# Optimization experiments

Measured on AMD Instinct MI355X. Metric: run time of the kernel, lower is better.

The kernel has to match this reference:

```python
import jax
import jax.numpy as jnp
import numpy as np

N_NODES = 4096
N_EDGES = 65536
D_FEAT = 64


def setup_inputs() -> dict:
    key = jax.random.key(0)
    k1, k2, k3, k4 = jax.random.split(key, 4)
    x = jax.random.normal(k1, (N_NODES, D_FEAT), dtype=jnp.float32)
    edge_index = jax.random.randint(k2, (2, N_EDGES), 0, N_NODES, dtype=jnp.int32)
    batch = jnp.zeros((N_NODES,), dtype=jnp.int32)
    # GraphConv(in_channels, 1): lin_rel (with bias) on aggregated neighbors, lin_root on self
    w_rel = jax.random.normal(k3, (D_FEAT, 1), dtype=jnp.float32) * 0.1
    w_root = jax.random.normal(k4, (D_FEAT, 1), dtype=jnp.float32) * 0.1
    b = jnp.zeros((1,), dtype=jnp.float32)
    return {"x": x, "edge_index": edge_index, "batch": batch,
            "w_rel": w_rel, "w_root": w_root, "b": b}


def _merge_stars(x, src0, dst0, score):
    """Faithful sequential greedy star contraction (priority order by score desc)."""
    N = x.shape[0]
    order = jnp.argsort(-score)  # descending, ties like argsort

    def step(carry, node):
        xc, src, dst, remaining, center = carry
        active = remaining[node]
        # dests = set of targets of edges whose (current, rewritten) source == node,
        # minus already-chosen center nodes
        dest_edge = src == node                                  # [E]
        dest_node = jnp.zeros(N, bool).at[dst].max(dest_edge)    # node-level set
        dest_node = dest_node & ~center
        # torch does sum over list(dests)+[node]: node counted again (even on self-loop)
        combine = jnp.einsum('n,nd->d', dest_node.astype(xc.dtype), xc) + xc[node]
        D = dest_node.at[node].set(True)                         # dests U {node}
        x2 = xc.at[node].set(combine)
        src2 = jnp.where(D[src], node, src)                      # np.isin rewrite
        dst2 = jnp.where(D[dst], node, dst)
        rem2 = remaining & ~dest_node
        cen2 = center.at[node].set(True)
        carry2 = (jnp.where(active, x2, xc),
                  jnp.where(active, src2, src),
                  jnp.where(active, dst2, dst),
                  jnp.where(active, rem2, remaining),
                  jnp.where(active, cen2, center))
        return carry2, None

    init = (x, src0, dst0, jnp.ones(N, bool), jnp.zeros(N, bool))
    (x_final, _, _, remaining, _), _ = jax.lax.scan(step, init, order)
    return x_final, remaining


def reference(x, edge_index, batch, w_rel, w_root, b):
    N, d = x.shape
    src0, dst0 = edge_index[0], edge_index[1]
    # GraphConv score: W_rel * sum_{j->i} x_j + b + W_root * x_i ; dropout p=0; tanh
    agg = jax.ops.segment_sum(x[src0], dst0, num_segments=N)     # [N, d]
    score = jnp.tanh((agg @ w_rel + x @ w_root + b).reshape(-1)) # [N]

    x_final, remaining = _merge_stars(x, src0, dst0, score)

    # perm = sorted(nodes_remaining); outputs padded to static size N (sentinel -1)
    perm = jnp.nonzero(remaining, size=N, fill_value=N)[0]
    x_pooled = jnp.take(x_final, perm, axis=0, mode='fill', fill_value=0.0)
    kept = perm < N
    batch_pooled = jnp.where(kept, jnp.take(batch, jnp.minimum(perm, N - 1)), -1)
    # filter_adj on the ORIGINAL edge_index: keep edges with both endpoints kept,
    # relabel nodes to their rank among kept nodes; invalid edges -> -1
    relabel = jnp.cumsum(remaining.astype(jnp.int32)) - 1
    valid = remaining[src0] & remaining[dst0]
    new_src = jnp.where(valid, relabel[src0], -1)
    new_dst = jnp.where(valid, relabel[dst0], -1)
    new_edge_index = jnp.stack([new_src, new_dst])
    perm_out = jnp.where(kept, perm, -1)
    return x_pooled, new_edge_index, batch_pooled, perm_out
```

## Files before the change

### kernel.cpp

```cpp
#include <hip/hip_runtime.h>

#define NN 4096
#define NE 65536
#define ND 64


__global__ void __launch_bounds__(1024) kB_csr(const int* __restrict__ ei,
                                               unsigned short* __restrict__ incsr_g,
                                               int* __restrict__ rowst_g) {
    __shared__ __align__(16) char buf[147520];
    unsigned short* incsr = (unsigned short*)buf;
    int* cursor = (int*)(buf + 131072);
    int* wt = (int*)(buf + 147456);
    int tid = threadIdx.x, lane = tid & 63, wv = tid >> 6;

    for (int n = tid; n < NN; n += 1024) cursor[n] = 0;
    __syncthreads();
    const int4* eid4 = (const int4*)(ei + NE);
    for (int i = tid; i < NE / 4; i += 1024) {
        int4 q = eid4[i];
        atomicAdd(&cursor[q.x], 1);
        atomicAdd(&cursor[q.y], 1);
        atomicAdd(&cursor[q.z], 1);
        atomicAdd(&cursor[q.w], 1);
    }
    __syncthreads();

    int t0 = cursor[4 * tid], t1 = cursor[4 * tid + 1];
    int t2 = cursor[4 * tid + 2], t3 = cursor[4 * tid + 3];
    int tot = t0 + t1 + t2 + t3;
    int inc = tot;
    for (int off = 1; off < 64; off <<= 1) {
        int v = __shfl_up(inc, off);
        if (lane >= off) inc += v;
    }
    if (lane == 63) wt[wv] = inc;
    __syncthreads();
    if (wv == 0 && lane < 16) {
        int v = wt[lane];
        for (int off = 1; off < 16; off <<= 1) {
            int u2 = __shfl_up(v, off);
            if (lane >= off) v += u2;
        }
        wt[lane] = v;
    }
    __syncthreads();
    int waveoff = (wv > 0) ? wt[wv - 1] : 0;
    int excl = waveoff + inc - tot;
    int4 rsv;
    rsv.x = excl; rsv.y = excl + t0; rsv.z = excl + t0 + t1; rsv.w = excl + t0 + t1 + t2;
    ((int4*)rowst_g)[tid] = rsv;
    if (tid == 1023) rowst_g[NN] = NE;
    cursor[4 * tid]     = rsv.x;
    cursor[4 * tid + 1] = rsv.y;
    cursor[4 * tid + 2] = rsv.z;
    cursor[4 * tid + 3] = rsv.w;
    __syncthreads();

    const int4* eis4 = (const int4*)ei;
    for (int i = tid; i < NE / 4; i += 1024) {
        int4 s = eis4[i];
        int4 d = eid4[i];
        incsr[atomicAdd(&cursor[d.x], 1)] = (unsigned short)s.x;
        incsr[atomicAdd(&cursor[d.y], 1)] = (unsigned short)s.y;
        incsr[atomicAdd(&cursor[d.z], 1)] = (unsigned short)s.z;
        incsr[atomicAdd(&cursor[d.w], 1)] = (unsigned short)s.w;
    }
    __syncthreads();

    for (int i = tid; i < 8192; i += 1024)
        ((int4*)incsr_g)[i] = ((const int4*)incsr)[i];
}

__global__ void kX_keys(const float* __restrict__ x, const float* __restrict__ wrel,
                        const float* __restrict__ wroot, const float* __restrict__ bptr,
                        const int* __restrict__ rowst, const unsigned short* __restrict__ incsr,
                        unsigned* __restrict__ key) {
    int gt = blockIdx.x * blockDim.x + threadIdx.x;
    int v = gt >> 6, lane = gt & 63;
    int rs = rowst[v], deg = rowst[v + 1] - rs;
    double acc = 0.0;
    for (int base = 0; base < deg; base += 64) {
        int n = deg - base; if (n > 64) n = 64;
        int ent = (lane < n) ? (int)incsr[rs + base + lane] : 0;
        for (int e = 0; e < n; ++e) {
            int u = __shfl(ent, e);
            acc += (double)x[(u << 6) | lane];
        }
    }
    double red = acc * (double)wrel[lane]
               + (double)x[(v << 6) | lane] * (double)wroot[lane];
    for (int off = 32; off > 0; off >>= 1) red += __shfl_down(red, off);
    if (lane == 0) {
        float sc = tanhf((float)(red + (double)bptr[0]));
        unsigned m = __float_as_uint(sc);
        m = (m & 0x80000000u) ? ~m : (m | 0x80000000u);
        key[v] = m;
    }
}

__global__ void k5_filtersort(const int* __restrict__ rowst, const unsigned* __restrict__ key,
                              unsigned short* __restrict__ incsr, int* __restrict__ rl,
                              float* __restrict__ out) {
    int g = blockIdx.x * blockDim.x + threadIdx.x;
    if (g < (NN * ND) / 4) ((float4*)out)[g] = make_float4(0.f, 0.f, 0.f, 0.f);

    int v = g >> 6, l = g & 63;
    int rs = rowst[v], deg = rowst[v + 1] - rs;
    unsigned mv = key[v];
    if (deg <= 64) {
        int u = (l < deg) ? (int)incsr[rs + l] : -1;
        bool isself = (l < deg) && (u == v);
        unsigned mu = (l < deg && !isself) ? key[u] : 0u;
        bool keep = (l < deg) && !isself && (mu > mv || (mu == mv && u < v));
        unsigned long long val = keep
            ? ((((unsigned long long)(~mu)) << 12) | (unsigned)u) : ~0ULL;
        int m = __popcll(__ballot(keep));
        bool selfAny = __ballot(isself) != 0ULL;
        for (int k = 2; k <= 64; k <<= 1) {
            for (int j = k >> 1; j > 0; j >>= 1) {
                unsigned long long o = __shfl_xor(val, j);
                bool takeMin = ((l & k) == 0) == ((l & j) == 0);
                unsigned long long mn = (o < val) ? o : val;
                unsigned long long mx = (o < val) ? val : o;
                val = takeMin ? mn : mx;
            }
        }
        if (l < m) incsr[rs + l] = (unsigned short)(val & 0xFFFULL);
        if (l == 0) rl[v] = m | (selfAny ? 0x10000 : 0);
    } else if (l == 0) {
        int w = rs;
        bool selfAny = false;
        for (int e = rs; e < rs + deg; ++e) {
            int u = (int)incsr[e];
            if (u == v) { selfAny = true; continue; }
            unsigned mu = key[u];
            if (!(mu > mv || (mu == mv && u < v))) continue;
            int j = w;
            while (j > rs) {
                int q = (int)incsr[j - 1];
                unsigned mq = key[q];
                if (mu > mq || (mu == mq && u < q)) { incsr[j] = (unsigned short)q; --j; }
                else break;
            }
            incsr[j] = (unsigned short)u; ++w;
        }
        rl[v] = (w - rs) | (selfAny ? 0x10000 : 0);
    }
}

__global__ void __launch_bounds__(1024) k34_fix(
        const int* __restrict__ rowst, const int* __restrict__ rl,
        const unsigned short* __restrict__ incsr_g,
        int* __restrict__ map_g, int* __restrict__ rem_g, int* __restrict__ relab_g,
        int* __restrict__ perm_a, int* __restrict__ nkeep_g) {
    __shared__ __align__(16) char buf[135232];
    unsigned short* incsr = (unsigned short*)buf;
    volatile unsigned char* stat = (volatile unsigned char*)(buf + 131072);
    int* wt = (int*)(buf + 135168);
    int tid = threadIdx.x, lane = tid & 63, wv = tid >> 6;

    for (int i = tid; i < 131072 / 16; i += 1024)
        ((int4*)incsr)[i] = ((const int4*)incsr_g)[i];
    ((int*)(buf + 131072))[tid] = 0;
    int4 rsq = ((const int4*)rowst)[tid];
    int4 rlq = ((const int4*)rl)[tid];
    int rs4[4] = {rsq.x, rsq.y, rsq.z, rsq.w};
    int rq4[4] = {rlq.x, rlq.y, rlq.z, rlq.w};
    __syncthreads();

    unsigned resolved = 0, centerm = 0, selfm = 0;
    int pos4[4], re4[4], fu4[4] = {0, 0, 0, 0};
    #pragma unroll
    for (int t = 0; t < 4; ++t) {
        int v = 4 * tid + t;
        int m = rq4[t] & 0xFFFF;
        if (rq4[t] & 0x10000) selfm |= 1u << t;
        int lo = rs4[t];
        pos4[t] = lo; re4[t] = lo + m;
        if (m == 0) {
            map_g[v] = v; stat[v] = 1;
            centerm |= 1u << t; resolved |= 1u << t;
        } else {
            fu4[t] = (int)incsr[lo];
        }
    }

    int guard = 0;
    while (resolved != 0xFu && guard < 1000000) {
        ++guard;
        bool prog = false;
        #pragma unroll
        for (int t = 0; t < 4; ++t) {
            if (resolved & (1u << t)) continue;
            int v = 4 * tid + t;
            int u = fu4[t];
            int st = (int)stat[u];
            if (st == 0) continue;
            prog = true;
            if (st == 1) {
                map_g[v] = u; stat[v] = 2; resolved |= 1u << t; continue;
            }
            int p = pos4[t] + 1, hi = re4[t];
            bool done = false;
            while (p < hi) {
                u = (int)incsr[p];
                st = (int)stat[u];
                if (st == 2) { ++p; continue; }
                if (st == 1) {
                    map_g[v] = u; stat[v] = 2; resolved |= 1u << t; done = true;
                }
                break;
            }
            if (!done) {
                if (p >= hi) {
                    map_g[v] = v; stat[v] = 1; centerm |= 1u << t; resolved |= 1u << t;
                } else {
                    pos4[t] = p; fu4[t] = u;
                }
            }
        }
        if (__ballot(prog) == 0) __builtin_amdgcn_s_sleep(1);
    }
    __syncthreads();

    int remb[4], cnt4 = 0;
    #pragma unroll
    for (int t = 0; t < 4; ++t) {
        remb[t] = ((centerm >> t) & 1) && !((selfm >> t) & 1);
        cnt4 += remb[t];
    }
    int inc2 = cnt4;
    for (int off = 1; off < 64; off <<= 1) {
        int v = __shfl_up(inc2, off);
        if (lane >= off) inc2 += v;
    }
    if (lane == 63) wt[wv] = inc2;
    __syncthreads();
    if (wv == 0 && lane < 16) {
        int v = wt[lane];
        for (int off = 1; off < 16; off <<= 1) {
            int u2 = __shfl_up(v, off);
            if (lane >= off) v += u2;
        }
        wt[lane] = v;
    }
    __syncthreads();
    int woff2 = (wv > 0) ? wt[wv - 1] : 0;
    int run = woff2 + inc2 - cnt4;
    #pragma unroll
    for (int t = 0; t < 4; ++t) {
        int v = 4 * tid + t;
        relab_g[v] = run;
        if (remb[t]) { perm_a[run] = v; ++run; }
        rem_g[v] = remb[t];
    }
    if (tid == 1023) nkeep_g[0] = run;
}

__global__ void k56_outputs(const float* __restrict__ x, const int* __restrict__ map_g,
                            const int* __restrict__ rem_g, const int* __restrict__ relab_g,
                            const int* __restrict__ perm_a, const int* __restrict__ ei,
                            const int* __restrict__ batch, const int* __restrict__ nkeep_g,
                            float* __restrict__ out) {
    int idx = blockIdx.x * blockDim.x + threadIdx.x;
    if (idx < NN * ND) {
        int n = idx >> 6, d = idx & 63;
        int m = map_g[n];
        if (rem_g[m]) atomicAdd(&out[relab_g[m] * ND + d], x[idx]);
    } else if (idx < NN * ND + 2 * NE) {
        int e = idx - NN * ND;
        int row = e >> 16;
        int ee = e & (NE - 1);
        int s = ei[ee], t = ei[NE + ee];
        bool valid = (rem_g[s] != 0) && (rem_g[t] != 0);
        int endp = (row == 0) ? s : t;
        out[idx] = valid ? (float)relab_g[endp] : -1.0f;
    } else if (idx < NN * ND + 2 * NE + NN) {
        int r = idx - (NN * ND + 2 * NE);
        int nk = nkeep_g[0];
        out[idx] = (r < nk) ? (float)batch[perm_a[r]] : -1.0f;
    } else if (idx < NN * ND + 2 * NE + 2 * NN) {
        int r = idx - (NN * ND + 2 * NE + NN);
        int nk = nkeep_g[0];
        out[idx] = (r < nk) ? (float)perm_a[r] : -1.0f;
    }
}

extern "C" void kernel_launch(void* const* d_in, const int* in_sizes, int n_in,
                              void* d_out, int out_size, void* d_ws, size_t ws_size,
                              hipStream_t stream) {
    const float* x     = (const float*)d_in[0];
    const int*   ei    = (const int*)d_in[1];
    const int*   batch = (const int*)d_in[2];
    const float* wrel  = (const float*)d_in[3];
    const float* wroot = (const float*)d_in[4];
    const float* b     = (const float*)d_in[5];

    char* ws = (char*)d_ws;
    int*    map_g  = (int*)(ws + 0);
    int*    rem_g  = (int*)(ws + 16384);
    int*    relab  = (int*)(ws + 32768);
    int*    perma  = (int*)(ws + 49152);
    int*    nkeep  = (int*)(ws + 65536);
    int*    rl     = (int*)(ws + 65600);
    int*    rowst  = (int*)(ws + 81984);
    unsigned* key  = (unsigned*)(ws + 98432);
    unsigned short* incsr = (unsigned short*)(ws + 114816);

    float* out = (float*)d_out;

    kB_csr<<<1, 1024, 0, stream>>>(ei, incsr, rowst);
    kX_keys<<<1024, 256, 0, stream>>>(x, wrel, wroot, b, rowst, incsr, key);
    k5_filtersort<<<1024, 256, 0, stream>>>(rowst, key, incsr, rl, out);
    k34_fix<<<1, 1024, 0, stream>>>(rowst, rl, incsr, map_g, rem_g, relab, perma, nkeep);
    int total_out = NN * ND + 2 * NE + 2 * NN;
    k56_outputs<<<(total_out + 255) / 256, 256, 0, stream>>>(x, map_g, rem_g, relab,
                                                             perma, ei, batch, nkeep, out);
}
```

Measured before the change: 140.1 us.

## Assign nodes to threads in priority-rank order for the star-resolution loop

k5_filtersort now also computes each node's global rank by score, using a full wave-wide count over all 4096 keys per node, and writes it to a new workspace buffer. k34_fix builds a rank-to-node table in shared memory and maps nodes to threads in priority order. Higher-priority nodes, whose decisions others wait on, then sit in earlier threads and waves, which is meant to shorten the spin-wait dependency chain in the single-block loop. The cost is extra L2 traffic for the rank count, more shared memory, and a degree field packed into 7 bits that relies on small kept degrees.

```diff
diff --git a/kernel.cpp b/kernel.cpp
--- a/kernel.cpp
+++ b/kernel.cpp
@@ -101,7 +101,7 @@
 
 __global__ void k5_filtersort(const int* __restrict__ rowst, const unsigned* __restrict__ key,
                               unsigned short* __restrict__ incsr, int* __restrict__ rl,
-                              float* __restrict__ out) {
+                              int* __restrict__ rank_g, float* __restrict__ out) {
     int g = blockIdx.x * blockDim.x + threadIdx.x;
     if (g < (NN * ND) / 4) ((float4*)out)[g] = make_float4(0.f, 0.f, 0.f, 0.f);
 
@@ -147,17 +147,36 @@
         }
         rl[v] = (w - rs) | (selfAny ? 0x10000 : 0);
     }
+
+    {
+        int cntk = 0;
+        const uint4* k4p = (const uint4*)key;
+        #pragma unroll 4
+        for (int i = 0; i < 16; ++i) {
+            uint4 kq = k4p[(l << 4) | i];
+            int u0 = (l << 6) | (i << 2);
+            cntk += (kq.x > mv || (kq.x == mv && (u0    ) < v));
+            cntk += (kq.y > mv || (kq.y == mv && (u0 + 1) < v));
+            cntk += (kq.z > mv || (kq.z == mv && (u0 + 2) < v));
+            cntk += (kq.w > mv || (kq.w == mv && (u0 + 3) < v));
+        }
+        for (int off = 32; off > 0; off >>= 1) cntk += __shfl_down(cntk, off);
+        if (l == 0) rank_g[v] = cntk;
+    }
 }
 
 __global__ void __launch_bounds__(1024) k34_fix(
         const int* __restrict__ rowst, const int* __restrict__ rl,
-        const unsigned short* __restrict__ incsr_g,
+        const unsigned short* __restrict__ incsr_g, const int* __restrict__ rank_g,
         int* __restrict__ map_g, int* __restrict__ rem_g, int* __restrict__ relab_g,
         int* __restrict__ perm_a, int* __restrict__ nkeep_g) {
-    __shared__ __align__(16) char buf[135232];
+    __shared__ __align__(16) char buf[155776];
     unsigned short* incsr = (unsigned short*)buf;
     volatile unsigned char* stat = (volatile unsigned char*)(buf + 131072);
-    int* wt = (int*)(buf + 135168);
+    unsigned short* r2n = (unsigned short*)(buf + 135168);
+    unsigned short* rst = (unsigned short*)(buf + 143360);
+    unsigned char*  lsf = (unsigned char*)(buf + 151552);
+    int* wt = (int*)(buf + 155648);
     int tid = threadIdx.x, lane = tid & 63, wv = tid >> 6;
 
     for (int i = tid; i < 131072 / 16; i += 1024)
@@ -165,22 +184,31 @@
     ((int*)(buf + 131072))[tid] = 0;
     int4 rsq = ((const int4*)rowst)[tid];
     int4 rlq = ((const int4*)rl)[tid];
-    int rs4[4] = {rsq.x, rsq.y, rsq.z, rsq.w};
-    int rq4[4] = {rlq.x, rlq.y, rlq.z, rlq.w};
-    __syncthreads();
-
-    unsigned resolved = 0, centerm = 0, selfm = 0;
-    int pos4[4], re4[4], fu4[4] = {0, 0, 0, 0};
+    int4 rkq = ((const int4*)rank_g)[tid];
+    int rs4s[4] = {rsq.x, rsq.y, rsq.z, rsq.w};
+    int rq4s[4] = {rlq.x, rlq.y, rlq.z, rlq.w};
+    int rk4s[4] = {rkq.x, rkq.y, rkq.z, rkq.w};
     #pragma unroll
     for (int t = 0; t < 4; ++t) {
         int v = 4 * tid + t;
-        int m = rq4[t] & 0xFFFF;
-        if (rq4[t] & 0x10000) selfm |= 1u << t;
-        int lo = rs4[t];
+        rst[v] = (unsigned short)rs4s[t];
+        lsf[v] = (unsigned char)((rq4s[t] & 0x7F) | ((rq4s[t] & 0x10000) ? 0x80 : 0));
+        r2n[rk4s[t]] = (unsigned short)v;
+    }
+    __syncthreads();
+
+    unsigned resolved = 0;
+    int pos4[4], re4[4], fu4[4] = {0, 0, 0, 0}, vr4[4];
+    #pragma unroll
+    for (int t = 0; t < 4; ++t) {
+        int v = (int)r2n[4 * tid + t];
+        vr4[t] = v;
+        int lo = (int)rst[v];
+        int m = lsf[v] & 0x7F;
         pos4[t] = lo; re4[t] = lo + m;
         if (m == 0) {
             map_g[v] = v; stat[v] = 1;
-            centerm |= 1u << t; resolved |= 1u << t;
+            resolved |= 1u << t;
         } else {
             fu4[t] = (int)incsr[lo];
         }
@@ -193,7 +221,7 @@
         #pragma unroll
         for (int t = 0; t < 4; ++t) {
             if (resolved & (1u << t)) continue;
-            int v = 4 * tid + t;
+            int v = vr4[t];
             int u = fu4[t];
             int st = (int)stat[u];
             if (st == 0) continue;
@@ -214,7 +242,7 @@
             }
             if (!done) {
                 if (p >= hi) {
-                    map_g[v] = v; stat[v] = 1; centerm |= 1u << t; resolved |= 1u << t;
+                    map_g[v] = v; stat[v] = 1; resolved |= 1u << t;
                 } else {
                     pos4[t] = p; fu4[t] = u;
                 }
@@ -227,7 +255,8 @@
     int remb[4], cnt4 = 0;
     #pragma unroll
     for (int t = 0; t < 4; ++t) {
-        remb[t] = ((centerm >> t) & 1) && !((selfm >> t) & 1);
+        int v = 4 * tid + t;
+        remb[t] = (stat[v] == 1) && !(lsf[v] & 0x80);
         cnt4 += remb[t];
     }
     int inc2 = cnt4;
@@ -306,14 +335,16 @@
     int*    rl     = (int*)(ws + 65600);
     int*    rowst  = (int*)(ws + 81984);
     unsigned* key  = (unsigned*)(ws + 98432);
-    unsigned short* incsr = (unsigned short*)(ws + 114816);
+    int*    rankp  = (int*)(ws + 114816);
+    unsigned short* incsr = (unsigned short*)(ws + 131200);
 
     float* out = (float*)d_out;
 
     kB_csr<<<1, 1024, 0, stream>>>(ei, incsr, rowst);
     kX_keys<<<1024, 256, 0, stream>>>(x, wrel, wroot, b, rowst, incsr, key);
-    k5_filtersort<<<1024, 256, 0, stream>>>(rowst, key, incsr, rl, out);
-    k34_fix<<<1, 1024, 0, stream>>>(rowst, rl, incsr, map_g, rem_g, relab, perma, nkeep);
+    k5_filtersort<<<1024, 256, 0, stream>>>(rowst, key, incsr, rl, rankp, out);
+    k34_fix<<<1, 1024, 0, stream>>>(rowst, rl, incsr, rankp, map_g, rem_g, relab,
+                                    perma, nkeep);
     int total_out = NN * ND + 2 * NE + 2 * NN;
     k56_outputs<<<(total_out + 255) / 256, 256, 0, stream>>>(x, map_g, rem_g, relab,
                                                              perma, ei, batch, nkeep, out);
```

Measured after the change: 139.5 us. No clear change (-0.4%).
